# Kernel optimization log

Measured on AMD Instinct MI355X. Metric: run time of the kernel, lower is better.

## Reference

```python
import math
import jax, jax.numpy as jnp
import numpy as np
from jax import lax

PI = math.pi

def _gauss1d(ks, sigma):
    # kornia gaussian: centered at (ks-1)/2 for both odd and even ks
    x = jnp.arange(ks, dtype=jnp.float32) - (ks - 1) / 2.0
    g = jnp.exp(-0.5 * (x / sigma) ** 2)
    return g / g.sum()

def _unfold_nonoverlap(x, k):
    # F.unfold(x, kernel_size=k, stride=k) for x (B,1,H,W), H,W divisible by k
    B, C, H, W = x.shape
    nH, nW = H // k, W // k
    p = x.reshape(B, nH, k, nW, k).transpose(0, 2, 4, 1, 3)
    return p.reshape(B, k * k, nH * nW)

def _sift(x, ps, nab=8, nsb=4, clipval=0.2, eps=1e-10):
    # kornia SIFTDescriptor(patch_size=ps), x: (N,1,ps,ps) -> (N,128)
    N = x.shape[0]
    g1 = _gauss1d(ps, ps / math.sqrt(2.0))
    gk = jnp.outer(g1, g1)  # (ps,ps), sum 1
    # spatial_gradient mode='diff', normalized, replicate pad
    xp = jnp.pad(x, ((0, 0), (0, 0), (0, 0), (1, 1)), mode='edge')
    gx = 0.5 * (xp[..., 2:] - xp[..., :-2])
    yp = jnp.pad(x, ((0, 0), (0, 0), (1, 1), (0, 0)), mode='edge')
    gy = 0.5 * (yp[:, :, 2:, :] - yp[:, :, :-2, :])
    mag = jnp.sqrt(gx * gx + gy * gy + eps) * gk  # (N,1,ps,ps)
    ori = jnp.arctan2(gy, gx + eps) + 2.0 * PI
    o_big = nab * ori / (2.0 * PI)
    bo0f = jnp.floor(o_big)
    w1 = o_big - bo0f
    bo0 = bo0f.astype(jnp.int32) % nab
    bo1 = (bo0 + 1) % nab
    c0 = jax.nn.one_hot(bo0[:, 0], nab, axis=1, dtype=x.dtype)  # (N,8,ps,ps)
    c1 = jax.nn.one_hot(bo1[:, 0], nab, axis=1, dtype=x.dtype)
    bins = c0 * ((1.0 - w1) * mag) + c1 * (w1 * mag)  # (N,8,ps,ps)
    # triangular pooling kernel, depthwise conv over the 8 angular bins
    bk = 2 * (ps // (nsb + 1)); stride = ps // nsb; pad = bk // 4
    half = bk / 2.0
    xc2 = half - jnp.abs(jnp.arange(bk, dtype=jnp.float32) + 0.5 - half)
    pk = jnp.outer(xc2, xc2) / (half * half)
    pk = jnp.tile(pk[None, None], (nab, 1, 1, 1))  # (8,1,bk,bk)
    pooled = lax.conv_general_dilated(bins, pk, (stride, stride),
        [(pad, pad), (pad, pad)], feature_group_count=nab,
        dimension_numbers=('NCHW', 'OIHW', 'NCHW'))  # (N,8,4,4)
    d = pooled.reshape(N, -1)
    d = d / jnp.maximum(jnp.linalg.norm(d, axis=1, keepdims=True), 1e-12)
    d = jnp.clip(d, 0.0, clipval)
    d = d / jnp.maximum(jnp.linalg.norm(d, axis=1, keepdims=True), 1e-12)
    d = jnp.sqrt(d / jnp.maximum(jnp.abs(d).sum(1, keepdims=True), 1e-12) + eps)  # rootsift
    return d

def _conv_t(x, w, b, stride=2, pad=1):
    # torch ConvTranspose2d; w: (Cin,Cout,k,k)
    k = w.shape[-1]
    wT = jnp.transpose(jnp.flip(w, (-2, -1)), (1, 0, 2, 3))  # (Cout,Cin,k,k)
    y = lax.conv_general_dilated(x, wT, (1, 1),
        [(k - 1 - pad, k - 1 - pad)] * 2, lhs_dilation=(stride, stride),
        dimension_numbers=('NCHW', 'OIHW', 'NCHW'))
    return y + b[None, :, None, None]

def _gn(x, groups, w, b, eps=1e-5):
    N, C, H, W = x.shape
    xg = x.reshape(N, groups, -1)
    mean = xg.mean(-1, keepdims=True)
    var = ((xg - mean) ** 2).mean(-1, keepdims=True)
    xn = ((xg - mean) * lax.rsqrt(var + eps)).reshape(N, C, H, W)
    return xn * w[None, :, None, None] + b[None, :, None, None]

def _jbf(x, guide, ky, kx, sigma_color, sy, sx):
    # kornia joint_bilateral_blur, border='reflect', color_distance='l1'
    B, C, H, W = x.shape
    py, px = ky // 2, kx // 2
    xp = jnp.pad(x, ((0, 0), (0, 0), (py, py), (px, px)), mode='reflect')
    gp = jnp.pad(guide, ((0, 0), (0, 0), (py, py), (px, px)), mode='reflect')
    def win(p):
        return jnp.stack([p[:, :, i:i + H, j:j + W] for i in range(ky) for j in range(kx)], axis=-1)
    ux, ug = win(xp), win(gp)  # (B,C,H,W,ky*kx)
    diff = ug - guide[..., None]
    cd2 = jnp.square(jnp.sum(jnp.abs(diff), axis=1, keepdims=True))
    ck = jnp.exp((-0.5 / (sigma_color ** 2)) * cd2)  # (B,1,H,W,K)
    sk = jnp.outer(_gauss1d(ky, sy), _gauss1d(kx, sx)).reshape(1, 1, 1, 1, -1)
    kern = sk * ck
    return (ux * kern).sum(-1) / kern.sum(-1)

def _forward(x, d1w, d1b, g1w, g1b, s1w, s1b, d2w, d2b, g2w, g2b, s2w, s2b,
             d3w, d3b, g3w, g3b, d4w, d4b, g4w, g4b, fw, fb):
    B = x.shape[0]
    s7 = _sift(_unfold_nonoverlap(x, 7).reshape(-1, 1, 32, 32), 32).reshape(B, 128, 7, 7)
    h = jax.nn.relu(_gn(_conv_t(s7, d1w, d1b), 8, g1w, g1b))  # (B,32,14,14); dropout=identity (eval)
    s14 = _sift(_unfold_nonoverlap(x, 14).reshape(-1, 1, 16, 16), 16).reshape(B, 128, 14, 14)
    sk1 = jnp.einsum('bchw,oc->bohw', s14, s1w[:, :, 0, 0]) + s1b[None, :, None, None]
    h = jax.nn.relu(_gn(_conv_t(jnp.concatenate([h, sk1], 1), d2w, d2b), 4, g2w, g2b))  # (B,16,28,28)
    s28 = _sift(_unfold_nonoverlap(x, 28).reshape(-1, 1, 8, 8), 8).reshape(B, 128, 28, 28)
    sk2 = jnp.einsum('bchw,oc->bohw', s28, s2w[:, :, 0, 0]) + s2b[None, :, None, None]
    h = jax.nn.relu(_gn(_conv_t(jnp.concatenate([h, sk2], 1), d3w, d3b), 2, g3w, g3b))  # (B,8,56,56)
    h = jax.nn.relu(_gn(_conv_t(h, d4w, d4b), 1, g4w, g4b))  # (B,4,112,112)
    h = _conv_t(h, fw, fb)  # (B,2,224,224)
    h = _jbf(h, jnp.tile(x, (1, 2, 1, 1)), 5, 5, 0.1, 1.5, 1.5)
    scale = jnp.array([0.436, 0.615], dtype=h.dtype)
    return jnp.tanh(h) * scale[None, :, None, None]

def setup_inputs() -> dict:
    key = jax.random.key(0)
    ks = jax.random.split(key, 8)
    B = 16
    f32 = jnp.float32
    def rn(k, shp, s=0.05):
        return jax.random.normal(k, shp, f32) * s
    return {
        'x': jax.random.uniform(ks[0], (B, 1, 224, 224), f32),
        'd1w': rn(ks[1], (128, 32, 4, 4)), 'd1b': jnp.zeros((32,), f32),
        'g1w': jnp.ones((32,), f32), 'g1b': jnp.zeros((32,), f32),
        's1w': rn(ks[2], (32, 128, 1, 1)), 's1b': jnp.zeros((32,), f32),
        'd2w': rn(ks[3], (64, 16, 4, 4)), 'd2b': jnp.zeros((16,), f32),
        'g2w': jnp.ones((16,), f32), 'g2b': jnp.zeros((16,), f32),
        's2w': rn(ks[4], (16, 128, 1, 1)), 's2b': jnp.zeros((16,), f32),
        'd3w': rn(ks[5], (32, 8, 4, 4)), 'd3b': jnp.zeros((8,), f32),
        'g3w': jnp.ones((8,), f32), 'g3b': jnp.zeros((8,), f32),
        'd4w': rn(ks[6], (8, 4, 4, 4)), 'd4b': jnp.zeros((4,), f32),
        'g4w': jnp.ones((4,), f32), 'g4b': jnp.zeros((4,), f32),
        'fw': rn(ks[7], (4, 2, 4, 4)), 'fb': jnp.zeros((2,), f32),
    }

def reference(x, d1w, d1b, g1w, g1b, s1w, s1b, d2w, d2b, g2w, g2b, s2w, s2b,
              d3w, d3b, g3w, g3b, d4w, d4b, g4w, g4b, fw, fb):
    return _forward(x, d1w, d1b, g1w, g1b, s1w, s1b, d2w, d2b, g2w, g2b, s2w, s2b,
                    d3w, d3b, g3w, g3b, d4w, d4b, g4w, g4b, fw, fb)
```

## Files before the change

kernel.cpp:

```cpp
#include <hip/hip_runtime.h>
#include <math.h>

#define PI_F 3.14159265358979323846f

template<int PS, int K, int NT>
__global__ __launch_bounds__(NT)
void sift_kernel(const float* __restrict__ x, float* __restrict__ out)
{
    constexpr int NPIX = PS*PS;
    constexpr int BK = 2*(PS/5);
    constexpr int STRIDE = PS/4;
    constexpr int PAD = BK/4;
    constexpr float HALF = BK*0.5f;
    constexpr int NWAVE = NT/64;
    constexpr int HALVES = (NT >= 256) ? 2 : 1;
    constexpr int ROWS = BK / HALVES;

    __shared__ float patch[NPIX];
    __shared__ float bins[8*NPIX];
    __shared__ float g1[PS];
    __shared__ float pool2[128];
    __shared__ float wred[NWAVE];
    __shared__ float gsum_s;

    const int tid = threadIdx.x;
    const int n = blockIdx.x;
    const int b = n / (K*K);
    const int c = n % (K*K);
    const int ki = c / K;
    const int kj = c % K;

    const float* xb = x + (size_t)b*224*224;
    for (int idx = tid; idx < NPIX; idx += NT) {
        int i = idx / PS, j = idx - i*PS;
        patch[idx] = xb[(i*K + ki)*224 + (j*K + kj)];
    }
    if (tid < PS) {
        const float sigma = (float)PS * 0.70710678118654752440f;
        float xv = (float)tid - (PS-1)*0.5f;
        float t = xv / sigma;
        g1[tid] = expf(-0.5f*t*t);
    }
    for (int idx = tid; idx < 8*NPIX; idx += NT) bins[idx] = 0.f;
    __syncthreads();
    if (tid == 0) {
        float s = 0.f;
        for (int i = 0; i < PS; i++) s += g1[i];
        gsum_s = s;
    }
    __syncthreads();
    const float ginv = 1.0f / (gsum_s*gsum_s);

    for (int idx = tid; idx < NPIX; idx += NT) {
        int i = idx / PS, j = idx - i*PS;
        int jm = j > 0 ? j-1 : 0, jp = j < PS-1 ? j+1 : PS-1;
        int im = i > 0 ? i-1 : 0, ip = i < PS-1 ? i+1 : PS-1;
        float gx = 0.5f*(patch[i*PS+jp] - patch[i*PS+jm]);
        float gy = 0.5f*(patch[ip*PS+j] - patch[im*PS+j]);
        float mag = sqrtf(gx*gx + gy*gy + 1e-10f) * (g1[i]*g1[j]*ginv);
        float ori = atan2f(gy, gx + 1e-10f) + 2.f*PI_F;
        float obig = ori * (8.f/(2.f*PI_F));
        float bo0f = floorf(obig);
        float w1 = obig - bo0f;
        int bo0 = ((int)bo0f) & 7;
        int bo1 = (bo0 + 1) & 7;
        bins[bo0*NPIX + idx] = (1.f - w1)*mag;
        bins[bo1*NPIX + idx] = w1*mag;
    }
    __syncthreads();

    float pacc = 0.f;
    const int t = tid & 127;
    const int half = (HALVES == 2) ? (tid >> 7) : 0;
    if (tid < 128*HALVES) {
        int o = t >> 4;
        int py = (t >> 2) & 3;
        int px = t & 3;
        int sy = py*STRIDE - PAD;
        int sx = px*STRIDE - PAD;
        const float* bo = bins + o*NPIX;
        for (int dr = 0; dr < ROWS; dr++) {
            int di = half*ROWS + dr;
            int i = sy + di;
            if (i < 0 || i >= PS) continue;
            float wi = HALF - fabsf((float)di + 0.5f - HALF);
            for (int dj = 0; dj < BK; dj++) {
                int j = sx + dj;
                if (j < 0 || j >= PS) continue;
                float wj = HALF - fabsf((float)dj + 0.5f - HALF);
                pacc += bo[i*PS + j] * (wi*wj);
            }
        }
    }
    if (HALVES == 2) {
        if (half == 1) pool2[t] = pacc;
        __syncthreads();
    }
    float d = 0.f;
    if (tid < 128) {
        d = pacc;
        if (HALVES == 2) d += pool2[tid];
        d *= 1.0f/(HALF*HALF);
    }

    const int wv = tid >> 6;
    const int ln = tid & 63;

    float v = d*d;
    #pragma unroll
    for (int off = 32; off > 0; off >>= 1) v += __shfl_down(v, off);
    if (ln == 0) wred[wv] = v;
    __syncthreads();
    float nrm = 0.f;
    #pragma unroll
    for (int w2 = 0; w2 < NWAVE; w2++) nrm += wred[w2];
    nrm = sqrtf(nrm);
    __syncthreads();
    d = d / fmaxf(nrm, 1e-12f);
    d = fminf(fmaxf(d, 0.f), 0.2f);

    v = d*d;
    #pragma unroll
    for (int off = 32; off > 0; off >>= 1) v += __shfl_down(v, off);
    if (ln == 0) wred[wv] = v;
    __syncthreads();
    nrm = 0.f;
    #pragma unroll
    for (int w2 = 0; w2 < NWAVE; w2++) nrm += wred[w2];
    nrm = sqrtf(nrm);
    __syncthreads();
    d = d / fmaxf(nrm, 1e-12f);

    v = d;
    #pragma unroll
    for (int off = 32; off > 0; off >>= 1) v += __shfl_down(v, off);
    if (ln == 0) wred[wv] = v;
    __syncthreads();
    float ssum = 0.f;
    #pragma unroll
    for (int w2 = 0; w2 < NWAVE; w2++) ssum += wred[w2];
    d = sqrtf(d / fmaxf(ssum, 1e-12f) + 1e-10f);

    if (tid < 128) out[(size_t)n*128 + tid] = d;
}

template<int CO, int S>
__global__ __launch_bounds__(256)
void conv1x1(const float* __restrict__ in, const float* __restrict__ w,
             const float* __restrict__ bias, float* __restrict__ out)
{
    __shared__ float wt[128*CO];
    const int tid = threadIdx.x;
    for (int i = tid; i < 128*CO; i += 256) {
        int c = i / CO, co = i - c*CO;
        wt[i] = w[co*128 + c];
    }
    __syncthreads();
    int idx = blockIdx.x*256 + tid;
    int s = idx % S; int r = idx / S;
    int co4 = r % (CO/4); int b = r / (CO/4);
    int co = co4*4;
    const float* ib = in + (size_t)b*128*S + s;
    float acc0 = bias[co], acc1 = bias[co+1], acc2 = bias[co+2], acc3 = bias[co+3];
    #pragma unroll 8
    for (int c = 0; c < 128; c++) {
        float v = ib[c*S];
        const float4 wv = *(const float4*)&wt[c*CO + co];
        acc0 += v*wv.x; acc1 += v*wv.y; acc2 += v*wv.z; acc3 += v*wv.w;
    }
    float* ob = out + ((size_t)b*CO + co)*S + s;
    ob[0] = acc0; ob[S] = acc1; ob[2*S] = acc2; ob[3*S] = acc3;
}

template<int CIN0, int CIN1, int COUT, int G, int HIN, int NCH, int RT, int NT,
         bool FUSE, int GIN, int NGIN, int NBLK_IN, int NBLK_OUT>
__global__ __launch_bounds__(NT)
void convt_tiled(const float* __restrict__ in0, const float* __restrict__ in1,
                 const float* __restrict__ w, const float* __restrict__ bias,
                 const float2* __restrict__ pst_in,
                 const float* __restrict__ gnw, const float* __restrict__ gnb,
                 float* __restrict__ out, float2* __restrict__ pst_out)
{
    constexpr int CIN = CIN0 + CIN1;
    constexpr int CG = COUT / G;
    constexpr int NGRP = NCH / CG;
    constexpr int CB = COUT / NCH;
    constexpr int H0 = 2*HIN;
    constexpr int SP = H0*H0;
    constexpr int HIN2 = HIN*HIN;
    constexpr int NR = RT/2 + 2;
    constexpr int WIN = HIN + 2;
    constexpr int TILE = CIN*NR*WIN;
    constexpr int WSTRIDE = CIN*NCH*4 + 4;
    constexpr int NPOS = RT*H0;
    constexpr int NWAVE = NT/64;

    __shared__ float tile[TILE];
    __shared__ float wl2[4*WSTRIDE];
    __shared__ float a_s[CIN0];
    __shared__ float b_s[CIN0];
    __shared__ float wpart[NWAVE][NGRP][2];

    const int tid = threadIdx.x;
    const int by = blockIdx.y;
    const int bx = blockIdx.x;
    const int b  = by / CB;
    const int cb = by - b*CB;
    const int c0 = cb*NCH;
    const int g0 = c0 / CG;
    const int r0 = bx * RT;
    const int row0 = r0/2 - 1;

    if constexpr (FUSE) {
        if (tid < CIN0) {
            int gi = tid / (CIN0/GIN);
            float s0 = 0.f, s1 = 0.f;
            for (int k = 0; k < NBLK_IN; k++) {
                float2 p = pst_in[((size_t)b*GIN + gi)*NBLK_IN + k];
                s0 += p.x; s1 += p.y;
            }
            float mean = s0 * (1.f/NGIN);
            float var  = s1 * (1.f/NGIN) - mean*mean;
            float inv  = rsqrtf(var + 1e-5f);
            float a = inv * gnw[tid];
            a_s[tid] = a;
            b_s[tid] = gnb[tid] - mean*a;
        }
        __syncthreads();
    }

    for (int idx = tid; idx < 4*CIN*NCH*4; idx += NT) {
        int k = idx & 3;
        int t2 = idx >> 2;
        int j = t2 % NCH; t2 /= NCH;
        int ci = t2 % CIN;
        int pq = t2 / CIN;
        int pA = pq >> 1, qA = pq & 1;
        int dy = pA + 2*(k>>1), dx = qA + 2*(k&1);
        wl2[pq*WSTRIDE + (ci*NCH + j)*4 + k] = w[(ci*COUT + c0 + j)*16 + dy*4 + dx];
    }

    const float* i0 = in0 + (size_t)b*CIN0*HIN2;
    for (int idx = tid; idx < TILE; idx += NT) {
        int c = idx % WIN;
        int t2 = idx / WIN;
        int r = t2 % NR;
        int ci = t2 / NR;
        int iy = row0 + r, ix = c - 1;
        float v = 0.f;
        if (iy >= 0 && iy < HIN && ix >= 0 && ix < HIN) {
            if (CIN1 == 0 || ci < CIN0) {
                v = i0[ci*HIN2 + iy*HIN + ix];
                if constexpr (FUSE) v = fmaxf(v*a_s[ci] + b_s[ci], 0.f);
            } else {
                v = in1[((size_t)b*CIN1 + (ci-CIN0))*HIN2 + iy*HIN + ix];
            }
        }
        tile[idx] = v;
    }
    __syncthreads();

    float acc[NCH];
    #pragma unroll
    for (int j = 0; j < NCH; j++) acc[j] = 0.f;

    const bool active = tid < NPOS;
    if (active) {
        int oy = r0 + tid / H0, ox = tid % H0;
        int pA = (oy+1)&1, qA = (ox+1)&1;
        int iyA = (oy+1-pA)>>1, ixA = (ox+1-qA)>>1;
        int rA = iyA - row0;
        int cA = ixA + 1;
        int toff = rA*WIN + cA;
        const float* wbase = wl2 + (pA*2+qA)*WSTRIDE;

        #pragma unroll
        for (int j = 0; j < NCH; j++) acc[j] = bias[c0 + j];

        #pragma unroll 4
        for (int ci = 0; ci < CIN; ci++) {
            const float* tp = tile + ci*(NR*WIN) + toff;
            float l0 = tp[0];
            float l1 = tp[-1];
            float l2 = tp[-WIN];
            float l3 = tp[-WIN-1];
            const float* wr = wbase + ci*NCH*4;
            #pragma unroll
            for (int j = 0; j < NCH; j++) {
                const float4 wv = *(const float4*)(wr + j*4);
                acc[j] += l0*wv.x + l1*wv.y + l2*wv.z + l3*wv.w;
            }
        }
        float* ob = out + ((size_t)b*COUT + c0)*SP + r0*H0 + tid;
        #pragma unroll
        for (int j = 0; j < NCH; j++) ob[j*SP] = acc[j];
    }

    const int wv = tid >> 6;
    const int ln = tid & 63;
    #pragma unroll
    for (int grp = 0; grp < NGRP; grp++) {
        float ps = 0.f, pq2 = 0.f;
        #pragma unroll
        for (int j = 0; j < CG; j++) {
            float v = active ? acc[grp*CG + j] : 0.f;
            ps += v; pq2 += v*v;
        }
        #pragma unroll
        for (int off = 32; off > 0; off >>= 1) {
            ps  += __shfl_down(ps,  off);
            pq2 += __shfl_down(pq2, off);
        }
        if (ln == 0) { wpart[wv][grp][0] = ps; wpart[wv][grp][1] = pq2; }
    }
    __syncthreads();
    if (tid < NGRP) {
        float s0 = 0.f, s1 = 0.f;
        #pragma unroll
        for (int w2 = 0; w2 < NWAVE; w2++) { s0 += wpart[w2][tid][0]; s1 += wpart[w2][tid][1]; }
        pst_out[((size_t)b*G + g0 + tid)*NBLK_OUT + bx] = make_float2(s0, s1);
    }
}

__global__ __launch_bounds__(256)
void convt_final_fused(const float* __restrict__ in, const float* __restrict__ w,
                       const float* __restrict__ bias,
                       const float2* __restrict__ pst_in,
                       const float* __restrict__ gnw, const float* __restrict__ gnb,
                       float* __restrict__ out)
{
    __shared__ float wl2[128];
    __shared__ float a_s[4], b_s[4], bl[2], mv[2];
    const int tid = threadIdx.x;
    const int b = blockIdx.y;
    if (tid < 128) {
        int k = tid & 3;
        int t = tid >> 2;
        int co = t & 1; t >>= 1;
        int ci = t & 3;
        int pq = t >> 2;
        int pA = pq >> 1, qA = pq & 1;
        int dy = pA + 2*(k>>1), dx = qA + 2*(k&1);
        wl2[tid] = w[(ci*2 + co)*16 + dy*4 + dx];
    }
    if (tid < 2) bl[tid] = bias[tid];
    if (tid < 64) {
        float s0 = 0.f, s1 = 0.f;
        for (int k = tid; k < 56; k += 64) {
            float2 p = pst_in[(size_t)b*56 + k];
            s0 += p.x; s1 += p.y;
        }
        #pragma unroll
        for (int off = 32; off > 0; off >>= 1) {
            s0 += __shfl_down(s0, off);
            s1 += __shfl_down(s1, off);
        }
        if (tid == 0) {
            float mean = s0 * (1.f/50176.f);
            float var  = s1 * (1.f/50176.f) - mean*mean;
            mv[0] = mean;
            mv[1] = rsqrtf(var + 1e-5f);
        }
    }
    __syncthreads();
    if (tid < 4) {
        float a = mv[1] * gnw[tid];
        a_s[tid] = a;
        b_s[tid] = gnb[tid] - mv[0]*a;
    }
    __syncthreads();

    int e = blockIdx.x*256 + tid;
    int oy = e / 224, ox = e - oy*224;
    int pA = (oy+1)&1, iyA = (oy+1-pA)>>1, iyB = iyA-1;
    int qA = (ox+1)&1, ixA = (ox+1-qA)>>1, ixB = ixA-1;
    float mYA = (iyA < 112) ? 1.f : 0.f;
    float mYB = (iyB >= 0)  ? 1.f : 0.f;
    float mXA = (ixA < 112) ? 1.f : 0.f;
    float mXB = (ixB >= 0)  ? 1.f : 0.f;
    float m0 = mYA*mXA, m1 = mYA*mXB, m2 = mYB*mXA, m3 = mYB*mXB;
    int iyAc = min(iyA, 111), iyBc = max(iyB, 0);
    int ixAc = min(ixA, 111), ixBc = max(ixB, 0);
    int oAA = iyAc*112 + ixAc, oAB = iyAc*112 + ixBc;
    int oBA = iyBc*112 + ixAc, oBB = iyBc*112 + ixBc;
    const float* wbase = wl2 + (pA*2+qA)*32;

    float acc0 = bl[0], acc1 = bl[1];
    const float* ib = in + (size_t)b*4*112*112;
    #pragma unroll
    for (int ci = 0; ci < 4; ci++) {
        const float* ip = ib + ci*112*112;
        float a = a_s[ci], bb = b_s[ci];
        float l0 = fmaxf(ip[oAA]*a + bb, 0.f);
        float l1 = fmaxf(ip[oAB]*a + bb, 0.f);
        float l2 = fmaxf(ip[oBA]*a + bb, 0.f);
        float l3 = fmaxf(ip[oBB]*a + bb, 0.f);
        float t0 = l0*m0, t1 = l1*m1, t2 = l2*m2, t3 = l3*m3;
        const float4 w0 = *(const float4*)(wbase + ci*8);
        const float4 w1 = *(const float4*)(wbase + ci*8 + 4);
        acc0 += t0*w0.x + t1*w0.y + t2*w0.z + t3*w0.w;
        acc1 += t0*w1.x + t1*w1.y + t2*w1.z + t3*w1.w;
    }
    float* ob = out + (size_t)b*2*50176 + e;
    ob[0] = acc0;
    ob[50176] = acc1;
}

__global__ __launch_bounds__(256)
void bilateral_tiled(const float* __restrict__ x, const float* __restrict__ pre,
                     float* __restrict__ out)
{
    const float g[5] = {0.1200783f, 0.2338817f, 0.2920800f, 0.2338817f, 0.1200783f};
    __shared__ float xs[400], p0s[400], p1s[400];

    const int tid = threadIdx.x;
    const int b = blockIdx.z;
    const int ty0 = blockIdx.y*16;
    const int tx0 = blockIdx.x*16;
    const float* xb = x + (size_t)b*50176;
    const float* p0 = pre + (size_t)b*2*50176;
    const float* p1 = p0 + 50176;

    for (int idx = tid; idx < 400; idx += 256) {
        int r = idx / 20, cc = idx - r*20;
        int gy = ty0 - 2 + r;  gy = gy < 0 ? -gy : (gy > 223 ? 446 - gy : gy);
        int gx = tx0 - 2 + cc; gx = gx < 0 ? -gx : (gx > 223 ? 446 - gx : gx);
        int o = gy*224 + gx;
        xs[idx]  = xb[o];
        p0s[idx] = p0[o];
        p1s[idx] = p1[o];
    }
    __syncthreads();

    int ly = tid >> 4, lx = tid & 15;
    int base = (ly+2)*20 + (lx+2);
    float center = xs[base];
    float wsum = 0.f, a0 = 0.f, a1 = 0.f;
    #pragma unroll
    for (int di = -2; di <= 2; di++){
        #pragma unroll
        for (int dj = -2; dj <= 2; dj++){
            int o = base + di*20 + dj;
            float dg = xs[o] - center;
            float wgt = g[di+2]*g[dj+2]*__expf(-200.f*dg*dg);
            wsum += wgt;
            a0 += wgt * p0s[o];
            a1 += wgt * p1s[o];
        }
    }
    float inv = 1.0f / wsum;
    int s = (ty0 + ly)*224 + (tx0 + lx);
    out[(size_t)(b*2)*50176 + s]     = tanhf(a0*inv)*0.436f;
    out[(size_t)(b*2+1)*50176 + s]   = tanhf(a1*inv)*0.615f;
}

extern "C" void kernel_launch(void* const* d_in, const int* in_sizes, int n_in,
                              void* d_out, int out_size, void* d_ws, size_t ws_size,
                              hipStream_t stream) {
    (void)in_sizes; (void)n_in; (void)out_size; (void)ws_size;
    const float* x   = (const float*)d_in[0];
    const float* d1w = (const float*)d_in[1];
    const float* d1b = (const float*)d_in[2];
    const float* g1w = (const float*)d_in[3];
    const float* g1b = (const float*)d_in[4];
    const float* s1w = (const float*)d_in[5];
    const float* s1b = (const float*)d_in[6];
    const float* d2w = (const float*)d_in[7];
    const float* d2b = (const float*)d_in[8];
    const float* g2w = (const float*)d_in[9];
    const float* g2b = (const float*)d_in[10];
    const float* s2w = (const float*)d_in[11];
    const float* s2b = (const float*)d_in[12];
    const float* d3w = (const float*)d_in[13];
    const float* d3b = (const float*)d_in[14];
    const float* g3w = (const float*)d_in[15];
    const float* g3b = (const float*)d_in[16];
    const float* d4w = (const float*)d_in[17];
    const float* d4b = (const float*)d_in[18];
    const float* g4w = (const float*)d_in[19];
    const float* g4b = (const float*)d_in[20];
    const float* fw  = (const float*)d_in[21];
    const float* fb  = (const float*)d_in[22];
    float* out = (float*)d_out;

    float* ws  = (float*)d_ws;
    float* s7  = ws;
    float* s14 = s7  + 100352;
    float* s28 = s14 + 401408;
    float* sk1 = s28 + 1605632;
    float* sk2 = sk1 + 100352;
    float* h1  = sk2 + 200704;
    float* h2  = h1  + 100352;
    float* h3  = h2  + 200704;
    float* h4  = h3  + 401408;
    float* pre = h4  + 802816;
    float2* pst1 = (float2*)(pre + 1605632);
    float2* pst2 = pst1 + 128;
    float2* pst3 = pst2 + 448;
    float2* pst4 = pst3 + 448;

    sift_kernel<32, 7, 256><<<784,   256, 0, stream>>>(x, s7);
    sift_kernel<16,14, 256><<<3136,  256, 0, stream>>>(x, s14);
    sift_kernel< 8,28, 128><<<12544, 128, 0, stream>>>(x, s28);

    conv1x1<32, 196><<<98,  256, 0, stream>>>(s14, s1w, s1b, sk1);
    conv1x1<16, 784><<<196, 256, 0, stream>>>(s28, s2w, s2b, sk2);

    convt_tiled<128, 0, 32, 8,  7, 4, 14, 256, false, 1, 1, 1, 1>
        <<<dim3(1, 16*8), 256, 0, stream>>>(s7, nullptr, d1w, d1b, nullptr, nullptr, nullptr, h1, pst1);
    convt_tiled< 32,32, 16, 4, 14, 8,  4, 128, true, 8, 784, 1, 7>
        <<<dim3(7, 16*2), 128, 0, stream>>>(h1, sk1, d2w, d2b, pst1, g1w, g1b, h2, pst2);
    convt_tiled< 16,16,  8, 2, 28, 8,  4, 256, true, 4, 3136, 7, 14>
        <<<dim3(14, 16), 256, 0, stream>>>(h2, sk2, d3w, d3b, pst2, g2w, g2b, h3, pst3);
    convt_tiled<  8, 0,  4, 1, 56, 4,  2, 256, true, 2, 12544, 14, 56>
        <<<dim3(56, 16), 256, 0, stream>>>(h3, nullptr, d4w, d4b, pst3, g3w, g3b, h4, pst4);

    convt_final_fused<<<dim3(196, 16), 256, 0, stream>>>(h4, fw, fb, pst4, g4w, g4b, pre);
    bilateral_tiled<<<dim3(14, 14, 16), 256, 0, stream>>>(x, pre, out);
}
```

Baseline: 247.5 us.

## Use one-wave-per-patch SIFT for 8x8 patches and fuse final convT into bilateral

Adds a specialized SIFT kernel for 8x8 patches in which each 64-lane wavefront handles one patch. Gradients, binning, pooling and normalisation are done with cross-lane shuffles instead of shared memory and block barriers. Separately, the final transposed convolution with its groupnorm and ReLU is fused into the bilateral filter kernel, which computes the pre-filter values for its 20x20 halo tile directly. This removes the intermediate buffer write and read and one launch, at the cost of recomputing halo pixels.

Result: no change. 250.7 us (+1.3%).

```diff
diff --git a/kernel.cpp b/kernel.cpp
--- a/kernel.cpp
+++ b/kernel.cpp
@@ -2,6 +2,81 @@
 #include <math.h>
 
 #define PI_F 3.14159265358979323846f
+
+__global__ __launch_bounds__(256)
+void sift8_wave(const float* __restrict__ x, float* __restrict__ out)
+{
+    const int tid = threadIdx.x;
+    const int l = tid & 63;
+    const int wv = tid >> 6;
+    const int n = blockIdx.x*4 + wv;
+    const int b = n / 784;
+    const int c = n % 784;
+    const int ki = c / 28, kj = c % 28;
+    const int i = l >> 3, j = l & 7;
+
+    const float* xb = x + (size_t)b*50176;
+    float v = xb[(i*28 + ki)*224 + (j*28 + kj)];
+
+    int lL = (j > 0) ? l-1 : l;
+    int lR = (j < 7) ? l+1 : l;
+    int lU = (i > 0) ? l-8 : l;
+    int lD = (i < 7) ? l+8 : l;
+    float pL = __shfl(v, lL);
+    float pR = __shfl(v, lR);
+    float pU = __shfl(v, lU);
+    float pD = __shfl(v, lD);
+    float gx = 0.5f*(pR - pL);
+    float gy = 0.5f*(pD - pU);
+
+    float ti = ((float)i - 3.5f) * (1.f/5.65685424949238f);
+    float tj = ((float)j - 3.5f) * (1.f/5.65685424949238f);
+    float wsp = __expf(-0.5f*(ti*ti + tj*tj));
+    float mag = sqrtf(gx*gx + gy*gy + 1e-10f) * wsp;
+    float ori = atan2f(gy, gx + 1e-10f) + 2.f*PI_F;
+    float obig = ori * (8.f/(2.f*PI_F));
+    float bo0f = floorf(obig);
+    float w1 = obig - bo0f;
+    int bo0 = ((int)bo0f) & 7;
+    int bo1 = (bo0 + 1) & 7;
+    float c0 = (1.f - w1)*mag;
+    float c1 = w1*mag;
+
+    const int t = ((i & 1) << 1) | (j & 1);
+    float d0 = 0.f, d1 = 0.f;
+    #pragma unroll
+    for (int o = 0; o < 8; o++) {
+        float val = (bo0 == o ? c0 : 0.f) + (bo1 == o ? c1 : 0.f);
+        val += __shfl_xor(val, 1);
+        val += __shfl_xor(val, 8);
+        if (o == 2*t)     d0 = val;
+        if (o == 2*t + 1) d1 = val;
+    }
+
+    float s = d0*d0 + d1*d1;
+    #pragma unroll
+    for (int off = 32; off > 0; off >>= 1) s += __shfl_xor(s, off);
+    float nrm = fmaxf(sqrtf(s), 1e-12f);
+    d0 /= nrm; d1 /= nrm;
+    d0 = fminf(fmaxf(d0, 0.f), 0.2f);
+    d1 = fminf(fmaxf(d1, 0.f), 0.2f);
+    s = d0*d0 + d1*d1;
+    #pragma unroll
+    for (int off = 32; off > 0; off >>= 1) s += __shfl_xor(s, off);
+    nrm = fmaxf(sqrtf(s), 1e-12f);
+    d0 /= nrm; d1 /= nrm;
+    s = d0 + d1;
+    #pragma unroll
+    for (int off = 32; off > 0; off >>= 1) s += __shfl_xor(s, off);
+    s = fmaxf(s, 1e-12f);
+    d0 = sqrtf(d0/s + 1e-10f);
+    d1 = sqrtf(d1/s + 1e-10f);
+
+    int cell = (i >> 1)*4 + (j >> 1);
+    float* ob = out + (size_t)n*128 + cell;
+    ob[(2*t)*16]     = d0;
+    ob[(2*t + 1)*16] = d1;
+}
 
 template<int PS, int K, int NT>
 __global__ __launch_bounds__(NT)
@@ -323,16 +398,22 @@
 }
 
 __global__ __launch_bounds__(256)
-void convt_final_fused(const float* __restrict__ in, const float* __restrict__ w,
-                       const float* __restrict__ bias,
-                       const float2* __restrict__ pst_in,
-                       const float* __restrict__ gnw, const float* __restrict__ gnb,
-                       float* __restrict__ out)
+void final_bilateral(const float* __restrict__ h4, const float* __restrict__ fw,
+                     const float* __restrict__ fb, const float2* __restrict__ pst_in,
+                     const float* __restrict__ gnw, const float* __restrict__ gnb,
+                     const float* __restrict__ x, float* __restrict__ out)
 {
+    const float g[5] = {0.1200783f, 0.2338817f, 0.2920800f, 0.2338817f, 0.1200783f};
+    __shared__ float xs[400], p0s[400], p1s[400];
     __shared__ float wl2[128];
     __shared__ float a_s[4], b_s[4], bl[2], mv[2];
+
     const int tid = threadIdx.x;
-    const int b = blockIdx.y;
+    const int b = blockIdx.z;
+    const int ty0 = blockIdx.y*16;
+    const int tx0 = blockIdx.x*16;
+    const float* xb = x + (size_t)b*50176;
+
     if (tid < 128) {
         int k = tid & 3;
         int t = tid >> 2;
@@ -341,21 +422,22 @@
         int pq = t >> 2;
         int pA = pq >> 1, qA = pq & 1;
         int dy = pA + 2*(k>>1), dx = qA + 2*(k&1);
-        wl2[tid] = w[(ci*2 + co)*16 + dy*4 + dx];
-    }
-    if (tid < 2) bl[tid] = bias[tid];
-    if (tid < 64) {
+        wl2[tid] = fw[(ci*2 + co)*16 + dy*4 + dx];
+    }
+    if (tid < 2) bl[tid] = fb[tid];
+    if (tid >= 192) {
+        int k0 = tid - 192;
         float s0 = 0.f, s1 = 0.f;
-        for (int k = tid; k < 56; k += 64) {
-            float2 p = pst_in[(size_t)b*56 + k];
-            s0 += p.x; s1 += p.y;
+        if (k0 < 56) {
+            float2 p = pst_in[(size_t)b*56 + k0];
+            s0 = p.x; s1 = p.y;
         }
         #pragma unroll
         for (int off = 32; off > 0; off >>= 1) {
             s0 += __shfl_down(s0, off);
             s1 += __shfl_down(s1, off);
         }
-        if (tid == 0) {
+        if (k0 == 0) {
             float mean = s0 * (1.f/50176.f);
             float var  = s1 * (1.f/50176.f) - mean*mean;
             mv[0] = mean;
@@ -370,65 +452,43 @@
     }
     __syncthreads();
 
-    int e = blockIdx.x*256 + tid;
-    int oy = e / 224, ox = e - oy*224;
-    int pA = (oy+1)&1, iyA = (oy+1-pA)>>1, iyB = iyA-1;
-    int qA = (ox+1)&1, ixA = (ox+1-qA)>>1, ixB = ixA-1;
-    float mYA = (iyA < 112) ? 1.f : 0.f;
-    float mYB = (iyB >= 0)  ? 1.f : 0.f;
-    float mXA = (ixA < 112) ? 1.f : 0.f;
-    float mXB = (ixB >= 0)  ? 1.f : 0.f;
-    float m0 = mYA*mXA, m1 = mYA*mXB, m2 = mYB*mXA, m3 = mYB*mXB;
-    int iyAc = min(iyA, 111), iyBc = max(iyB, 0);
-    int ixAc = min(ixA, 111), ixBc = max(ixB, 0);
-    int oAA = iyAc*112 + ixAc, oAB = iyAc*112 + ixBc;
-    int oBA = iyBc*112 + ixAc, oBB = iyBc*112 + ixBc;
-    const float* wbase = wl2 + (pA*2+qA)*32;
-
-    float acc0 = bl[0], acc1 = bl[1];
-    const float* ib = in + (size_t)b*4*112*112;
-    #pragma unroll
-    for (int ci = 0; ci < 4; ci++) {
-        const float* ip = ib + ci*112*112;
-        float a = a_s[ci], bb = b_s[ci];
-        float l0 = fmaxf(ip[oAA]*a + bb, 0.f);
-        float l1 = fmaxf(ip[oAB]*a + bb, 0.f);
-        float l2 = fmaxf(ip[oBA]*a + bb, 0.f);
-        float l3 = fmaxf(ip[oBB]*a + bb, 0.f);
-        float t0 = l0*m0, t1 = l1*m1, t2 = l2*m2, t3 = l3*m3;
-        const float4 w0 = *(const float4*)(wbase + ci*8);
-        const float4 w1 = *(const float4*)(wbase + ci*8 + 4);
-        acc0 += t0*w0.x + t1*w0.y + t2*w0.z + t3*w0.w;
-        acc1 += t0*w1.x + t1*w1.y + t2*w1.z + t3*w1.w;
-    }
-    float* ob = out + (size_t)b*2*50176 + e;
-    ob[0] = acc0;
-    ob[50176] = acc1;
-}
-
-__global__ __launch_bounds__(256)
-void bilateral_tiled(const float* __restrict__ x, const float* __restrict__ pre,
-                     float* __restrict__ out)
-{
-    const float g[5] = {0.1200783f, 0.2338817f, 0.2920800f, 0.2338817f, 0.1200783f};
-    __shared__ float xs[400], p0s[400], p1s[400];
-
-    const int tid = threadIdx.x;
-    const int b = blockIdx.z;
-    const int ty0 = blockIdx.y*16;
-    const int tx0 = blockIdx.x*16;
-    const float* xb = x + (size_t)b*50176;
-    const float* p0 = pre + (size_t)b*2*50176;
-    const float* p1 = p0 + 50176;
-
+    const float* ib = h4 + (size_t)b*4*12544;
     for (int idx = tid; idx < 400; idx += 256) {
         int r = idx / 20, cc = idx - r*20;
-        int gy = ty0 - 2 + r;  gy = gy < 0 ? -gy : (gy > 223 ? 446 - gy : gy);
-        int gx = tx0 - 2 + cc; gx = gx < 0 ? -gx : (gx > 223 ? 446 - gx : gx);
-        int o = gy*224 + gx;
-        xs[idx]  = xb[o];
-        p0s[idx] = p0[o];
-        p1s[idx] = p1[o];
+        int oy = ty0 - 2 + r;  oy = oy < 0 ? -oy : (oy > 223 ? 446 - oy : oy);
+        int ox = tx0 - 2 + cc; ox = ox < 0 ? -ox : (ox > 223 ? 446 - ox : ox);
+        xs[idx] = xb[oy*224 + ox];
+
+        int pA = (oy+1)&1, iyA = (oy+1-pA)>>1, iyB = iyA-1;
+        int qA = (ox+1)&1, ixA = (ox+1-qA)>>1, ixB = ixA-1;
+        float mYA = (iyA < 112) ? 1.f : 0.f;
+        float mYB = (iyB >= 0)  ? 1.f : 0.f;
+        float mXA = (ixA < 112) ? 1.f : 0.f;
+        float mXB = (ixB >= 0)  ? 1.f : 0.f;
+        float m0 = mYA*mXA, m1 = mYA*mXB, m2 = mYB*mXA, m3 = mYB*mXB;
+        int iyAc = min(iyA, 111), iyBc = max(iyB, 0);
+        int ixAc = min(ixA, 111), ixBc = max(ixB, 0);
+        int oAA = iyAc*112 + ixAc, oAB = iyAc*112 + ixBc;
+        int oBA = iyBc*112 + ixAc, oBB = iyBc*112 + ixBc;
+        const float* wbase = wl2 + (pA*2+qA)*32;
+
+        float acc0 = bl[0], acc1 = bl[1];
+        #pragma unroll
+        for (int ci = 0; ci < 4; ci++) {
+            const float* ip = ib + ci*12544;
+            float a = a_s[ci], bb = b_s[ci];
+            float l0 = fmaxf(ip[oAA]*a + bb, 0.f);
+            float l1 = fmaxf(ip[oAB]*a + bb, 0.f);
+            float l2 = fmaxf(ip[oBA]*a + bb, 0.f);
+            float l3 = fmaxf(ip[oBB]*a + bb, 0.f);
+            float t0 = l0*m0, t1 = l1*m1, t2 = l2*m2, t3 = l3*m3;
+            const float4 w0 = *(const float4*)(wbase + ci*8);
+            const float4 w1 = *(const float4*)(wbase + ci*8 + 4);
+            acc0 += t0*w0.x + t1*w0.y + t2*w0.z + t3*w0.w;
+            acc1 += t0*w1.x + t1*w1.y + t2*w1.z + t3*w1.w;
+        }
+        p0s[idx] = acc0;
+        p1s[idx] = acc1;
     }
     __syncthreads();
 
@@ -493,15 +553,14 @@
     float* h2  = h1  + 100352;
     float* h3  = h2  + 200704;
     float* h4  = h3  + 401408;
-    float* pre = h4  + 802816;
-    float2* pst1 = (float2*)(pre + 1605632);
+    float2* pst1 = (float2*)(h4 + 802816);
     float2* pst2 = pst1 + 128;
     float2* pst3 = pst2 + 448;
     float2* pst4 = pst3 + 448;
 
     sift_kernel<32, 7, 256><<<784,   256, 0, stream>>>(x, s7);
     sift_kernel<16,14, 256><<<3136,  256, 0, stream>>>(x, s14);
-    sift_kernel< 8,28, 128><<<12544, 128, 0, stream>>>(x, s28);
+    sift8_wave<<<3136, 256, 0, stream>>>(x, s28);
 
     conv1x1<32, 196><<<98,  256, 0, stream>>>(s14, s1w, s1b, sk1);
     conv1x1<16, 784><<<196, 256, 0, stream>>>(s28, s2w, s2b, sk2);
@@ -515,6 +574,5 @@
     convt_tiled<  8, 0,  4, 1, 56, 4,  2, 256, true, 2, 12544, 14, 56>
         <<<dim3(56, 16), 256, 0, stream>>>(h3, nullptr, d4w, d4b, pst3, g3w, g3b, h4, pst4);
 
-    convt_final_fused<<<dim3(196, 16), 256, 0, stream>>>(h4, fw, fb, pst4, g4w, g4b, pre);
-    bilateral_tiled<<<dim3(14, 14, 16), 256, 0, stream>>>(x, pre, out);
+    final_bilateral<<<dim3(14, 14, 16), 256, 0, stream>>>(h4, fw, fb, pst4, g4w, g4b, x, out);
 }
```
